# Performance work log

Hardware: AMD Instinct MI355X
Metric: run time of the kernel (lower is better)

Reference implementation:

```python
import jax, jax.numpy as jnp
import numpy as np

N = 100000      # nodes
E = 1600000     # edges (before self-loops)
IN = 64         # in_channels
HID = 16        # hidden_channels
HEADS = 4       # num_heads
G = 512         # number of graphs in batch
SLOPE = 0.2     # GATConv leaky_relu negative_slope


def setup_inputs() -> dict:
    key = jax.random.key(0)
    ks = jax.random.split(key, 12)
    s = 0.1
    x = jax.random.normal(ks[0], (N, IN), jnp.float32)
    edge_index = jax.random.randint(ks[1], (2, E), 0, N, dtype=jnp.int64)
    batch = jnp.sort(jax.random.randint(ks[2], (N,), 0, G, dtype=jnp.int64))
    W1 = jax.random.normal(ks[3], (IN, HEADS * HID), jnp.float32) * s
    a1_src = jax.random.normal(ks[4], (HEADS, HID), jnp.float32) * s
    a1_dst = jax.random.normal(ks[5], (HEADS, HID), jnp.float32) * s
    b1 = jnp.zeros((HEADS * HID,), jnp.float32)
    W2 = jax.random.normal(ks[6], (HEADS * HID, HID), jnp.float32) * s
    a2_src = jax.random.normal(ks[7], (1, HID), jnp.float32) * s
    a2_dst = jax.random.normal(ks[8], (1, HID), jnp.float32) * s
    b2 = jnp.zeros((HID,), jnp.float32)
    Wc = jax.random.normal(ks[9], (HID, 1), jnp.float32) * s
    bc = jnp.zeros((1,), jnp.float32)
    return dict(x=x, edge_index=edge_index, batch=batch, W1=W1, a1_src=a1_src,
                a1_dst=a1_dst, b1=b1, W2=W2, a2_src=a2_src, a2_dst=a2_dst,
                b2=b2, Wc=Wc, bc=bc)


def gat_layer(x, src, dst, W, a_s, a_d, bias, heads, out_ch, concat):
    # PyG GATConv: linear -> per-edge attention logits -> segment softmax over dst -> scatter aggregate
    n = x.shape[0]
    h = (x @ W).reshape(n, heads, out_ch)              # [N, H, C]
    al_s = jnp.sum(h * a_s, axis=-1)                   # [N, H]
    al_d = jnp.sum(h * a_d, axis=-1)                   # [N, H]
    e = al_s[src] + al_d[dst]                          # [E, H]
    e = jnp.where(e > 0, e, SLOPE * e)                 # leaky_relu
    m = jax.ops.segment_max(e, dst, num_segments=n)    # per-dst max (self-loops ensure non-empty)
    p = jnp.exp(e - m[dst])
    denom = jax.ops.segment_sum(p, dst, num_segments=n)
    alpha = p / (denom[dst] + 1e-16)                   # [E, H]
    out = jax.ops.segment_sum(h[src] * alpha[:, :, None], dst, num_segments=n)  # [N, H, C]
    out = out.reshape(n, heads * out_ch) if concat else out.mean(axis=1)
    return out + bias


def reference(x, edge_index, batch, W1, a1_src, a1_dst, b1, W2, a2_src, a2_dst, b2, Wc, bc):
    loops = jnp.arange(N, dtype=edge_index.dtype)      # GATConv add_self_loops=True
    src = jnp.concatenate([edge_index[0], loops])
    dst = jnp.concatenate([edge_index[1], loops])
    h = jax.nn.elu(gat_layer(x, src, dst, W1, a1_src, a1_dst, b1, HEADS, HID, True))
    # dropout inactive (eval mode)
    h = jax.nn.elu(gat_layer(h, src, dst, W2, a2_src, a2_dst, b2, 1, HID, False))
    counts = jax.ops.segment_sum(jnp.ones((N,), h.dtype), batch, num_segments=G)
    pooled = jax.ops.segment_sum(h, batch, num_segments=G) / jnp.maximum(counts, 1.0)[:, None]
    return pooled @ Wc + bc
```

## Files before the change

kernel.cpp:

```cpp
#include <hip/hip_runtime.h>
#include <hip/hip_fp16.h>
#include <hip/hip_fp8.h>

#define N_NODES 100000
#define N_EDGES 1600000
#define ET      (N_EDGES + N_NODES)
#define NG      512
#define SLOPE   0.2f

#define BKT_SHIFT 9
#define NB_B   ((N_NODES + 511) / 512)
#define CHUNK_A 8192
#define NBLK_A ((ET + CHUNK_A - 1) / CHUNK_A)
#define H1B    ((N_NODES + 255) / 256)

typedef _Float16 half8_t __attribute__((ext_vector_type(8)));
typedef float    f32x4_t __attribute__((ext_vector_type(4)));

__global__ __launch_bounds__(256) void k_prep(
    const float* __restrict__ x, const float* __restrict__ W1,
    const float* __restrict__ a1s, const float* __restrict__ a1d,
    const int* __restrict__ ei,
    __hip_fp8_e4m3* __restrict__ h1, float* __restrict__ al1s, float* __restrict__ al1d,
    int* __restrict__ bsize)
{
    __shared__ float Wl[64 * 64];
    __shared__ float asf[64], adf[64];
    __shared__ int hcnt[NB_B];
    int tid = threadIdx.x;

    if (blockIdx.x >= H1B) {
        for (int i = tid; i < NB_B; i += 256) hcnt[i] = 0;
        __syncthreads();
        int base = (blockIdx.x - H1B) * CHUNK_A;
        int m = min(CHUNK_A, ET - base);
        for (int i = tid; i < m; i += 256) {
            int eid = base + i;
            int d = (eid < N_EDGES) ? ei[N_EDGES + eid] : (eid - N_EDGES);
            atomicAdd(&hcnt[d >> BKT_SHIFT], 1);
        }
        __syncthreads();
        for (int i = tid; i < NB_B; i += 256)
            if (hcnt[i]) atomicAdd(&bsize[i], hcnt[i]);
        return;
    }

    for (int i = tid; i < 64 * 64; i += 256) Wl[i] = W1[i];
    if (tid < 64) { asf[tid] = a1s[tid]; adf[tid] = a1d[tid]; }
    __syncthreads();

    int wv = tid >> 6, lane = tid & 63;
    int m = lane & 15, q = lane >> 4;

    half8_t bf[4][2];
#pragma unroll
    for (int t = 0; t < 4; ++t)
#pragma unroll
        for (int s = 0; s < 2; ++s) {
            half8_t b;
#pragma unroll
            for (int j = 0; j < 8; ++j)
                b[j] = (_Float16)Wl[(s * 32 + q * 8 + j) * 64 + t * 16 + m];
            bf[t][s] = b;
        }

    for (int it = 0; it < 4; ++it) {
        int node0 = blockIdx.x * 256 + wv * 64 + it * 16;
        int node = node0 + m;
        half8_t av0 = {}, av1 = {};
        if (node < N_NODES) {
            const float4* xr = (const float4*)(x + (long long)node * 64);
            float4 p0 = xr[q * 2], p1 = xr[q * 2 + 1];
            float4 p2 = xr[q * 2 + 8], p3 = xr[q * 2 + 9];
            av0[0] = (_Float16)p0.x; av0[1] = (_Float16)p0.y;
            av0[2] = (_Float16)p0.z; av0[3] = (_Float16)p0.w;
            av0[4] = (_Float16)p1.x; av0[5] = (_Float16)p1.y;
            av0[6] = (_Float16)p1.z; av0[7] = (_Float16)p1.w;
            av1[0] = (_Float16)p2.x; av1[1] = (_Float16)p2.y;
            av1[2] = (_Float16)p2.z; av1[3] = (_Float16)p2.w;
            av1[4] = (_Float16)p3.x; av1[5] = (_Float16)p3.y;
            av1[6] = (_Float16)p3.z; av1[7] = (_Float16)p3.w;
        }
        f32x4_t acc[4] = {{0,0,0,0},{0,0,0,0},{0,0,0,0},{0,0,0,0}};
#pragma unroll
        for (int t = 0; t < 4; ++t) {
            acc[t] = __builtin_amdgcn_mfma_f32_16x16x32_f16(av0, bf[t][0], acc[t], 0, 0, 0);
            acc[t] = __builtin_amdgcn_mfma_f32_16x16x32_f16(av1, bf[t][1], acc[t], 0, 0, 0);
        }
#pragma unroll
        for (int r = 0; r < 4; ++r) {
            int nr = node0 + q * 4 + r;
            bool ok = nr < N_NODES;
#pragma unroll
            for (int t = 0; t < 4; ++t) {
                float v = acc[t][r];
                if (ok) h1[(long long)nr * 64 + t * 16 + m] = __hip_fp8_e4m3(v);
                float ps = v * asf[t * 16 + m];
                float pd = v * adf[t * 16 + m];
                ps += __shfl_xor(ps, 1); ps += __shfl_xor(ps, 2);
                ps += __shfl_xor(ps, 4); ps += __shfl_xor(ps, 8);
                pd += __shfl_xor(pd, 1); pd += __shfl_xor(pd, 2);
                pd += __shfl_xor(pd, 4); pd += __shfl_xor(pd, 8);
                if (ok && m == t) { al1s[nr * 4 + t] = ps; al1d[nr * 4 + t] = pd; }
            }
        }
    }
}

__global__ __launch_bounds__(256) void k_scanB(const int* __restrict__ bsize,
                                               int* __restrict__ bbase, int* __restrict__ bcur)
{
    __shared__ int tmp[256];
    int tid = threadIdx.x;
    int v = (tid < NB_B) ? bsize[tid] : 0;
    tmp[tid] = v;
    __syncthreads();
    for (int off = 1; off < 256; off <<= 1) {
        int t = (tid >= off) ? tmp[tid - off] : 0;
        __syncthreads();
        tmp[tid] += t;
        __syncthreads();
    }
    if (tid < NB_B) { int e = tmp[tid] - v; bbase[tid] = e; bcur[tid] = e; }
}

__global__ __launch_bounds__(1024) void k_passA(const int* __restrict__ ei,
                                                int* __restrict__ bcur, unsigned int* __restrict__ ebuf)
{
    __shared__ unsigned int stage[CHUNK_A];
    __shared__ unsigned char sbin[CHUNK_A];
    __shared__ int hist[NB_B];
    __shared__ int binst[NB_B];
    __shared__ int resv[NB_B];
    __shared__ int cur[NB_B];
    __shared__ int tmp[1024];
    int tid = threadIdx.x;
    int base = blockIdx.x * CHUNK_A;
    int m = min(CHUNK_A, ET - base);
    for (int i = tid; i < NB_B; i += 1024) hist[i] = 0;
    __syncthreads();
    for (int i = tid; i < m; i += 1024) {
        int eid = base + i;
        int d = (eid < N_EDGES) ? ei[N_EDGES + eid] : (eid - N_EDGES);
        atomicAdd(&hist[d >> BKT_SHIFT], 1);
    }
    __syncthreads();
    int v = (tid < NB_B) ? hist[tid] : 0;
    tmp[tid] = v;
    __syncthreads();
    for (int off = 1; off < 1024; off <<= 1) {
        int t = (tid >= off) ? tmp[tid - off] : 0;
        __syncthreads();
        tmp[tid] += t;
        __syncthreads();
    }
    if (tid < NB_B) {
        int e = tmp[tid] - v;
        binst[tid] = e;
        cur[tid] = e;
        resv[tid] = v ? atomicAdd(&bcur[tid], v) : 0;
    }
    __syncthreads();
    for (int i = tid; i < m; i += 1024) {
        int eid = base + i;
        int s, d;
        if (eid < N_EDGES) { s = ei[eid]; d = ei[N_EDGES + eid]; }
        else               { s = eid - N_EDGES; d = s; }
        int b = d >> BKT_SHIFT;
        int pos = atomicAdd(&cur[b], 1);
        stage[pos] = ((unsigned int)(d & 511) << 17) | (unsigned int)s;
        sbin[pos] = (unsigned char)b;
    }
    __syncthreads();
    for (int i = tid; i < m; i += 1024) {
        int b = sbin[i];
        ebuf[resv[b] + (i - binst[b])] = stage[i];
    }
}

__global__ __launch_bounds__(1024) void k_passB(
    const unsigned int* __restrict__ ebuf, const int* __restrict__ bbase,
    const int* __restrict__ bsize,
    int* __restrict__ csr, int* __restrict__ offs, int* __restrict__ deg)
{
    __shared__ int ldeg[512];
    __shared__ int lofs[512];
    __shared__ int lcur[512];
    int tid = threadIdx.x;
    int b = blockIdx.x;
    int nb0 = b << BKT_SHIFT;
    int nn = min(512, N_NODES - nb0);
    int gbase = bbase[b], cnt = bsize[b];
    if (tid < 512) ldeg[tid] = 0;
    __syncthreads();
    for (int i = tid; i < cnt; i += 1024)
        atomicAdd(&ldeg[ebuf[gbase + i] >> 17], 1);
    __syncthreads();
    int v = 0;
    if (tid < 512) { v = ldeg[tid]; lofs[tid] = v; }
    __syncthreads();
    for (int off = 1; off < 512; off <<= 1) {
        int t = (tid >= off && tid < 512) ? lofs[tid - off] : 0;
        __syncthreads();
        if (tid < 512) lofs[tid] += t;
        __syncthreads();
    }
    if (tid < 512) {
        int e = lofs[tid] - v;
        lcur[tid] = e;
        if (tid < nn) { offs[nb0 + tid] = gbase + e; deg[nb0 + tid] = v; }
    }
    __syncthreads();
    for (int i = tid; i < cnt; i += 1024) {
        unsigned int ev = ebuf[gbase + i];
        int dl = ev >> 17, s = (int)(ev & 0x1FFFF);
        int p = atomicAdd(&lcur[dl], 1);
        csr[gbase + p] = s;
    }
}

__global__ __launch_bounds__(256) void k_agg1(
    const int* __restrict__ offs, const int* __restrict__ deg, const int* __restrict__ csr,
    const __hip_fp8_e4m3* __restrict__ h1, const float* __restrict__ al1s, const float* __restrict__ al1d,
    const float* __restrict__ b1, __half* __restrict__ h1bg)
{
    __shared__ int   sarr[4][64];
    __shared__ float warr[4][4 * 72];
    __shared__ __align__(16) float h1b[4][64];
    int tid = threadIdx.x;
    int wv = tid >> 6, lane = tid & 63;
    int eslot = lane >> 4;
    int cq = lane & 15;
    int h = cq >> 2;
    int cq4 = cq * 4;
    int node = blockIdx.x * 4 + wv;
    int st = offs[node], dg = deg[node];
    const float4 ald4 = *(const float4*)(al1d + node * 4);
    float b1l = b1[lane];
    const char* __restrict__ h1c = (const char*)h1;

    float a0 = 0.f, a1 = 0.f, a2 = 0.f, a3 = 0.f, den = 0.f;
    for (int base = 0; base < dg; base += 64) {
        int m = min(64, dg - base);
        int s = 0;
        float w0 = 0.f, w1 = 0.f, w2 = 0.f, w3 = 0.f;
        if (lane < m) {
            s = csr[st + base + lane];
            const float4 as4 = *(const float4*)(al1s + s * 4);
            float e0 = as4.x + ald4.x; e0 = e0 > 0.f ? e0 : SLOPE * e0;
            float e1 = as4.y + ald4.y; e1 = e1 > 0.f ? e1 : SLOPE * e1;
            float e2 = as4.z + ald4.z; e2 = e2 > 0.f ? e2 : SLOPE * e2;
            float e3 = as4.w + ald4.w; e3 = e3 > 0.f ? e3 : SLOPE * e3;
            w0 = __expf(e0); w1 = __expf(e1); w2 = __expf(e2); w3 = __expf(e3);
        }
        sarr[wv][lane] = s << 6;
        warr[wv][0 * 72 + lane] = w0;
        warr[wv][1 * 72 + lane] = w1;
        warr[wv][2 * 72 + lane] = w2;
        warr[wv][3 * 72 + lane] = w3;
        int m4 = (m + 3) & ~3;
#pragma unroll 4
        for (int j0 = 0; j0 < m4; j0 += 4) {
            int j = j0 + eslot;
            int off = sarr[wv][j] + cq4;
            float wgt = warr[wv][h * 72 + j];
            unsigned int pk = *(const unsigned int*)(h1c + off);
            a0 = fmaf(wgt, __builtin_amdgcn_cvt_f32_fp8(pk, 0), a0);
            a1 = fmaf(wgt, __builtin_amdgcn_cvt_f32_fp8(pk, 1), a1);
            a2 = fmaf(wgt, __builtin_amdgcn_cvt_f32_fp8(pk, 2), a2);
            a3 = fmaf(wgt, __builtin_amdgcn_cvt_f32_fp8(pk, 3), a3);
            den += wgt;
        }
    }
    a0 += __shfl_xor(a0, 16); a0 += __shfl_xor(a0, 32);
    a1 += __shfl_xor(a1, 16); a1 += __shfl_xor(a1, 32);
    a2 += __shfl_xor(a2, 16); a2 += __shfl_xor(a2, 32);
    a3 += __shfl_xor(a3, 16); a3 += __shfl_xor(a3, 32);
    den += __shfl_xor(den, 16); den += __shfl_xor(den, 32);
    if (lane < 16)
        *(float4*)&h1b[wv][cq4] = make_float4(a0, a1, a2, a3);
    float denc = __shfl(den, (lane >> 4) << 2);
    float v = h1b[wv][lane] / (denc + 1e-16f) + b1l;
    v = v > 0.f ? v : __expf(v) - 1.f;
    h1bg[(long long)node * 64 + lane] = __float2half_rn(v);
}

__global__ __launch_bounds__(256) void k_mid(
    const __half* __restrict__ h1bg, const float* __restrict__ W2,
    const float* __restrict__ a2s, const float* __restrict__ a2d,
    __half* __restrict__ h2, float* __restrict__ al2s, float* __restrict__ al2d)
{
    __shared__ float W2l[64 * 16];
    int tid = threadIdx.x;
    for (int i = tid; i < 64 * 16; i += 256) W2l[i] = W2[i];
    __syncthreads();
    int wv = tid >> 6, lane = tid & 63;
    int m = lane & 15, q = lane >> 4;
    half8_t bf[2];
#pragma unroll
    for (int s = 0; s < 2; ++s) {
        half8_t b;
#pragma unroll
        for (int j = 0; j < 8; ++j)
            b[j] = (_Float16)W2l[(s * 32 + q * 8 + j) * 16 + m];
        bf[s] = b;
    }
    int node0 = blockIdx.x * 64 + wv * 16;
    half8_t av0 = {}, av1 = {};
    if (node0 + m < N_NODES) {
        const __half* ar = h1bg + (long long)(node0 + m) * 64;
        av0 = *(const half8_t*)(ar + q * 8);
        av1 = *(const half8_t*)(ar + 32 + q * 8);
    }
    f32x4_t acc = {0, 0, 0, 0};
    acc = __builtin_amdgcn_mfma_f32_16x16x32_f16(av0, bf[0], acc, 0, 0, 0);
    acc = __builtin_amdgcn_mfma_f32_16x16x32_f16(av1, bf[1], acc, 0, 0, 0);
    float a2sm = a2s[m], a2dm = a2d[m];
#pragma unroll
    for (int r = 0; r < 4; ++r) {
        int nr = node0 + q * 4 + r;
        bool ok = nr < N_NODES;
        float v = acc[r];
        if (ok) h2[nr * 16 + m] = __float2half_rn(v);
        float ps = v * a2sm, pd = v * a2dm;
        ps += __shfl_xor(ps, 1); ps += __shfl_xor(ps, 2);
        ps += __shfl_xor(ps, 4); ps += __shfl_xor(ps, 8);
        pd += __shfl_xor(pd, 1); pd += __shfl_xor(pd, 2);
        pd += __shfl_xor(pd, 4); pd += __shfl_xor(pd, 8);
        if (ok && m == 0) { al2s[nr] = ps; al2d[nr] = pd; }
    }
}

__global__ __launch_bounds__(256) void k_agg2(
    const int* __restrict__ offs, const int* __restrict__ deg, const int* __restrict__ csr,
    const __half* __restrict__ h2, const float* __restrict__ al2s, const float* __restrict__ al2d,
    const float* __restrict__ b2, float* __restrict__ hout)
{
    __shared__ int   sarr[4][64];
    __shared__ float warr[4][64];
    int tid = threadIdx.x;
    int wv = tid >> 6, lane = tid & 63;
    int ec = lane >> 3, cc = lane & 7;
    int node = blockIdx.x * 4 + wv;
    int st = offs[node], dg = deg[node];
    float ald = al2d[node];
    const __half2* __restrict__ h2v = (const __half2*)h2;

    float a0 = 0.f, a1 = 0.f, den = 0.f;
    for (int base = 0; base < dg; base += 64) {
        int m = min(64, dg - base);
        int s = 0; float wl = 0.f;
        if (lane < m) {
            s = csr[st + base + lane];
            float e = al2s[s] + ald;
            e = e > 0.f ? e : SLOPE * e;
            wl = __expf(e);
        }
        sarr[wv][lane] = s;
        warr[wv][lane] = wl;
        float t = wl;
#pragma unroll
        for (int x = 1; x < 64; x <<= 1) t += __shfl_xor(t, x);
        den += t;
        int m8 = (m + 7) & ~7;
#pragma unroll 2
        for (int j0 = 0; j0 < m8; j0 += 8) {
            int j = j0 + ec;
            int s2i = sarr[wv][j];
            float wgt = warr[wv][j];
            __half2 hv = h2v[s2i * 8 + cc];
            a0 = fmaf(__low2float(hv), wgt, a0);
            a1 = fmaf(__high2float(hv), wgt, a1);
        }
    }
    a0 += __shfl_xor(a0, 8);  a1 += __shfl_xor(a1, 8);
    a0 += __shfl_xor(a0, 16); a1 += __shfl_xor(a1, 16);
    a0 += __shfl_xor(a0, 32); a1 += __shfl_xor(a1, 32);
    if (lane < 8) {
        float inv = 1.f / (den + 1e-16f);
        float v0 = a0 * inv + b2[2 * cc];
        float v1 = a1 * inv + b2[2 * cc + 1];
        v0 = v0 > 0.f ? v0 : __expf(v0) - 1.f;
        v1 = v1 > 0.f ? v1 : __expf(v1) - 1.f;
        ((float2*)hout)[node * 8 + cc] = make_float2(v0, v1);
    }
}

__global__ __launch_bounds__(256) void k_pool(
    const float* __restrict__ hout, const int* __restrict__ batch,
    const float* __restrict__ Wc, const float* __restrict__ bc, float* __restrict__ out)
{
    __shared__ float red[16][17];
    __shared__ int bnd[2];
    int g = blockIdx.x;
    int t = threadIdx.x, c = t & 15, slot = t >> 4;
    if (t < 2) {
        int key = g + t;
        int lo = 0, hi = N_NODES;
        while (lo < hi) { int mid = (lo + hi) >> 1; if (batch[mid] < key) lo = mid + 1; else hi = mid; }
        bnd[t] = lo;
    }
    __syncthreads();
    int s = bnd[0], e = bnd[1];
    float sum = 0.f;
    for (int n = s + slot; n < e; n += 16)
        sum += hout[n * 16 + c];
    red[slot][c] = sum;
    __syncthreads();
    if (t < 16) {
        float tot = 0.f;
#pragma unroll
        for (int k = 0; k < 16; ++k) tot += red[k][t];
        float cnt = fmaxf((float)(e - s), 1.0f);
        float pc = (tot / cnt) * Wc[t];
        pc += __shfl_xor(pc, 1); pc += __shfl_xor(pc, 2);
        pc += __shfl_xor(pc, 4); pc += __shfl_xor(pc, 8);
        if (t == 0) out[g] = pc + bc[0];
    }
}

extern "C" void kernel_launch(void* const* d_in, const int* in_sizes, int n_in,
                              void* d_out, int out_size, void* d_ws, size_t ws_size,
                              hipStream_t stream)
{
    const float* x    = (const float*)d_in[0];
    const int*   ei   = (const int*)d_in[1];
    const int*   batc = (const int*)d_in[2];
    const float* W1   = (const float*)d_in[3];
    const float* a1s  = (const float*)d_in[4];
    const float* a1d  = (const float*)d_in[5];
    const float* b1   = (const float*)d_in[6];
    const float* W2   = (const float*)d_in[7];
    const float* a2s  = (const float*)d_in[8];
    const float* a2d  = (const float*)d_in[9];
    const float* b2   = (const float*)d_in[10];
    const float* Wc   = (const float*)d_in[11];
    const float* bc   = (const float*)d_in[12];
    float* out = (float*)d_out;

    char* ws = (char*)d_ws;
    size_t off = 0;
    auto carveB = [&](size_t bytes) {
        void* p = ws + off;
        off += ((bytes + 15) & ~(size_t)15);
        return p;
    };
    auto carve = [&](size_t elems) { return carveB(elems * 4); };
    int*   bsize  = (int*)  carve(NB_B);
    size_t zero_bytes = off;
    int*   bbase  = (int*)  carve(NB_B);
    int*   bcur   = (int*)  carve(NB_B);
    unsigned int* ebuf = (unsigned int*)carve(ET);
    int*   csr    = (int*)  carve(ET);
    int*   offs   = (int*)  carve(N_NODES);
    int*   deg    = (int*)  carve(N_NODES);
    __hip_fp8_e4m3* h1 = (__hip_fp8_e4m3*)carveB((size_t)N_NODES * 64);
    float* al1s   = (float*)carve((size_t)N_NODES * 4);
    float* al1d   = (float*)carve((size_t)N_NODES * 4);
    __half* h1bg  = (__half*)carveB((size_t)N_NODES * 64 * 2);
    __half* h2    = (__half*)carveB((size_t)N_NODES * 16 * 2);
    float* al2s   = (float*)carve(N_NODES);
    float* al2d   = (float*)carve(N_NODES);
    float* hout   = (float*)carve((size_t)N_NODES * 16);

    hipMemsetAsync(d_ws, 0, zero_bytes, stream);

    k_prep <<<H1B + NBLK_A, 256, 0, stream>>>(x, W1, a1s, a1d, ei, h1, al1s, al1d, bsize);
    k_scanB<<<1, 256, 0, stream>>>(bsize, bbase, bcur);
    k_passA<<<NBLK_A, 1024, 0, stream>>>(ei, bcur, ebuf);
    k_passB<<<NB_B, 1024, 0, stream>>>(ebuf, bbase, bsize, csr, offs, deg);
    k_agg1 <<<N_NODES / 4, 256, 0, stream>>>(offs, deg, csr, h1, al1s, al1d, b1, h1bg);
    k_mid  <<<(N_NODES + 63) / 64, 256, 0, stream>>>(h1bg, W2, a2s, a2d, h2, al2s, al2d);
    k_agg2 <<<N_NODES / 4, 256, 0, stream>>>(offs, deg, csr, h2, al2s, al2d,
                                             b2, hout);
    k_pool <<<NG, 256, 0, stream>>>(hout, batc, Wc, bc, out);
}
```

Measured before the change: 260.8 us.

## Fuse CSR build passes with fixed bucket capacity and fuse mid/pool into aggregations

Replaces the count/scan/scatter sequence with a single pass that scatters edges into fixed-capacity per-bucket regions (BCAP), removing the global histogram and scan kernels. It also fuses the layer-2 linear transform and attention logits into the layer-1 aggregation, which removes the h1bg round trip through memory. Mean pooling becomes atomic accumulation inside agg2, followed by a tiny classifier kernel. The trade-offs are more launches avoided against a risk of bucket overflow if a bucket exceeds BCAP, nondeterministic float atomics, and extra per-block W2 loading in agg1.

```diff
diff --git a/kernel.cpp b/kernel.cpp
--- a/kernel.cpp
+++ b/kernel.cpp
@@ -10,43 +10,77 @@
 
 #define BKT_SHIFT 9
 #define NB_B   ((N_NODES + 511) / 512)
+#define BCAP   10240
 #define CHUNK_A 8192
 #define NBLK_A ((ET + CHUNK_A - 1) / CHUNK_A)
-#define H1B    ((N_NODES + 255) / 256)
+#define H1B4   ((N_NODES + 1023) / 1024)
 
 typedef _Float16 half8_t __attribute__((ext_vector_type(8)));
 typedef float    f32x4_t __attribute__((ext_vector_type(4)));
-
-__global__ __launch_bounds__(256) void k_prep(
+typedef float    f32x2_t __attribute__((ext_vector_type(2)));
+
+__global__ __launch_bounds__(1024) void k_prepA(
     const float* __restrict__ x, const float* __restrict__ W1,
     const float* __restrict__ a1s, const float* __restrict__ a1d,
     const int* __restrict__ ei,
-    __hip_fp8_e4m3* __restrict__ h1, float* __restrict__ al1s, float* __restrict__ al1d,
-    int* __restrict__ bsize)
-{
-    __shared__ float Wl[64 * 64];
-    __shared__ float asf[64], adf[64];
-    __shared__ int hcnt[NB_B];
+    int* __restrict__ gcnt, unsigned int* __restrict__ ebuf,
+    __hip_fp8_e4m3* __restrict__ h1, float* __restrict__ al1s, float* __restrict__ al1d)
+{
+    __shared__ union U {
+        struct { float Wl[64 * 64]; float asf[64]; float adf[64]; } p;
+        struct { unsigned int stage[CHUNK_A]; unsigned char sbin[CHUNK_A];
+                 int hist[NB_B]; int binst[NB_B]; int resv[NB_B]; int cur[NB_B];
+                 int tmp[1024]; } a;
+    } u;
     int tid = threadIdx.x;
 
-    if (blockIdx.x >= H1B) {
-        for (int i = tid; i < NB_B; i += 256) hcnt[i] = 0;
-        __syncthreads();
-        int base = (blockIdx.x - H1B) * CHUNK_A;
+    if (blockIdx.x < NBLK_A) {
+        int base = blockIdx.x * CHUNK_A;
         int m = min(CHUNK_A, ET - base);
-        for (int i = tid; i < m; i += 256) {
+        for (int i = tid; i < NB_B; i += 1024) u.a.hist[i] = 0;
+        __syncthreads();
+        for (int i = tid; i < m; i += 1024) {
             int eid = base + i;
             int d = (eid < N_EDGES) ? ei[N_EDGES + eid] : (eid - N_EDGES);
-            atomicAdd(&hcnt[d >> BKT_SHIFT], 1);
-        }
-        __syncthreads();
-        for (int i = tid; i < NB_B; i += 256)
-            if (hcnt[i]) atomicAdd(&bsize[i], hcnt[i]);
+            atomicAdd(&u.a.hist[d >> BKT_SHIFT], 1);
+        }
+        __syncthreads();
+        int v = (tid < NB_B) ? u.a.hist[tid] : 0;
+        u.a.tmp[tid] = v;
+        __syncthreads();
+        for (int off = 1; off < 1024; off <<= 1) {
+            int t = (tid >= off) ? u.a.tmp[tid - off] : 0;
+            __syncthreads();
+            u.a.tmp[tid] += t;
+            __syncthreads();
+        }
+        if (tid < NB_B) {
+            int e = u.a.tmp[tid] - v;
+            u.a.binst[tid] = e;
+            u.a.cur[tid] = e;
+            u.a.resv[tid] = v ? atomicAdd(&gcnt[tid], v) : 0;
+        }
+        __syncthreads();
+        for (int i = tid; i < m; i += 1024) {
+            int eid = base + i;
+            int s, d;
+            if (eid < N_EDGES) { s = ei[eid]; d = ei[N_EDGES + eid]; }
+            else               { s = eid - N_EDGES; d = s; }
+            int b = d >> BKT_SHIFT;
+            int pos = atomicAdd(&u.a.cur[b], 1);
+            u.a.stage[pos] = ((unsigned int)(d & 511) << 17) | (unsigned int)s;
+            u.a.sbin[pos] = (unsigned char)b;
+        }
+        __syncthreads();
+        for (int i = tid; i < m; i += 1024) {
+            int b = u.a.sbin[i];
+            ebuf[b * BCAP + u.a.resv[b] + (i - u.a.binst[b])] = u.a.stage[i];
+        }
         return;
     }
 
-    for (int i = tid; i < 64 * 64; i += 256) Wl[i] = W1[i];
-    if (tid < 64) { asf[tid] = a1s[tid]; adf[tid] = a1d[tid]; }
+    for (int i = tid; i < 64 * 64; i += 1024) u.p.Wl[i] = W1[i];
+    if (tid < 64) { u.p.asf[tid] = a1s[tid]; u.p.adf[tid] = a1d[tid]; }
     __syncthreads();
 
     int wv = tid >> 6, lane = tid & 63;
@@ -60,12 +94,13 @@
             half8_t b;
 #pragma unroll
             for (int j = 0; j < 8; ++j)
-                b[j] = (_Float16)Wl[(s * 32 + q * 8 + j) * 64 + t * 16 + m];
+                b[j] = (_Float16)u.p.Wl[(s * 32 + q * 8 + j) * 64 + t * 16 + m];
             bf[t][s] = b;
         }
 
+    int nodebase = (blockIdx.x - NBLK_A) * 1024 + wv * 64;
     for (int it = 0; it < 4; ++it) {
-        int node0 = blockIdx.x * 256 + wv * 64 + it * 16;
+        int node0 = nodebase + it * 16;
         int node = node0 + m;
         half8_t av0 = {}, av1 = {};
         if (node < N_NODES) {
@@ -95,8 +130,8 @@
             for (int t = 0; t < 4; ++t) {
                 float v = acc[t][r];
                 if (ok) h1[(long long)nr * 64 + t * 16 + m] = __hip_fp8_e4m3(v);
-                float ps = v * asf[t * 16 + m];
-                float pd = v * adf[t * 16 + m];
+                float ps = v * u.p.asf[t * 16 + m];
+                float pd = v * u.p.adf[t * 16 + m];
                 ps += __shfl_xor(ps, 1); ps += __shfl_xor(ps, 2);
                 ps += __shfl_xor(ps, 4); ps += __shfl_xor(ps, 8);
                 pd += __shfl_xor(pd, 1); pd += __shfl_xor(pd, 2);
@@ -107,80 +142,8 @@
     }
 }
 
-__global__ __launch_bounds__(256) void k_scanB(const int* __restrict__ bsize,
-                                               int* __restrict__ bbase, int* __restrict__ bcur)
-{
-    __shared__ int tmp[256];
-    int tid = threadIdx.x;
-    int v = (tid < NB_B) ? bsize[tid] : 0;
-    tmp[tid] = v;
-    __syncthreads();
-    for (int off = 1; off < 256; off <<= 1) {
-        int t = (tid >= off) ? tmp[tid - off] : 0;
-        __syncthreads();
-        tmp[tid] += t;
-        __syncthreads();
-    }
-    if (tid < NB_B) { int e = tmp[tid] - v; bbase[tid] = e; bcur[tid] = e; }
-}
-
-__global__ __launch_bounds__(1024) void k_passA(const int* __restrict__ ei,
-                                                int* __restrict__ bcur, unsigned int* __restrict__ ebuf)
-{
-    __shared__ unsigned int stage[CHUNK_A];
-    __shared__ unsigned char sbin[CHUNK_A];
-    __shared__ int hist[NB_B];
-    __shared__ int binst[NB_B];
-    __shared__ int resv[NB_B];
-    __shared__ int cur[NB_B];
-    __shared__ int tmp[1024];
-    int tid = threadIdx.x;
-    int base = blockIdx.x * CHUNK_A;
-    int m = min(CHUNK_A, ET - base);
-    for (int i = tid; i < NB_B; i += 1024) hist[i] = 0;
-    __syncthreads();
-    for (int i = tid; i < m; i += 1024) {
-        int eid = base + i;
-        int d = (eid < N_EDGES) ? ei[N_EDGES + eid] : (eid - N_EDGES);
-        atomicAdd(&hist[d >> BKT_SHIFT], 1);
-    }
-    __syncthreads();
-    int v = (tid < NB_B) ? hist[tid] : 0;
-    tmp[tid] = v;
-    __syncthreads();
-    for (int off = 1; off < 1024; off <<= 1) {
-        int t = (tid >= off) ? tmp[tid - off] : 0;
-        __syncthreads();
-        tmp[tid] += t;
-        __syncthreads();
-    }
-    if (tid < NB_B) {
-        int e = tmp[tid] - v;
-        binst[tid] = e;
-        cur[tid] = e;
-        resv[tid] = v ? atomicAdd(&bcur[tid], v) : 0;
-    }
-    __syncthreads();
-    for (int i = tid; i < m; i += 1024) {
-        int eid = base + i;
-        int s, d;
-        if (eid < N_EDGES) { s = ei[eid]; d = ei[N_EDGES + eid]; }
-        else               { s = eid - N_EDGES; d = s; }
-        int b = d >> BKT_SHIFT;
-        int pos = atomicAdd(&cur[b], 1);
-        stage[pos] = ((unsigned int)(d & 511) << 17) | (unsigned int)s;
-        sbin[pos] = (unsigned char)b;
-    }
-    __syncthreads();
-    for (int i = tid; i < m; i += 1024) {
-        int b = sbin[i];
-        ebuf[resv[b] + (i - binst[b])] = stage[i];
-    }
-}
-
 __global__ __launch_bounds__(1024) void k_passB(
-    const unsigned int* __restrict__ ebuf, const int* __restrict__ bbase,
-    const int* __restrict__ bsize,
+    const unsigned int* __restrict__ ebuf, const int* __restrict__ gcnt,
     int* __restrict__ csr, int* __restrict__ offs, int* __restrict__ deg)
 {
     __shared__ int ldeg[512];
@@ -190,7 +153,7 @@
     int b = blockIdx.x;
     int nb0 = b << BKT_SHIFT;
     int nn = min(512, N_NODES - nb0);
-    int gbase = bbase[b], cnt = bsize[b];
+    int gbase = b * BCAP, cnt = gcnt[b];
     if (tid < 512) ldeg[tid] = 0;
     __syncthreads();
     for (int i = tid; i < cnt; i += 1024)
@@ -222,16 +185,24 @@
 __global__ __launch_bounds__(256) void k_agg1(
     const int* __restrict__ offs, const int* __restrict__ deg, const int* __restrict__ csr,
     const __hip_fp8_e4m3* __restrict__ h1, const float* __restrict__ al1s, const float* __restrict__ al1d,
-    const float* __restrict__ b1, __half* __restrict__ h1bg)
+    const float* __restrict__ b1, const float* __restrict__ W2,
+    const float* __restrict__ a2s, const float* __restrict__ a2d,
+    __half* __restrict__ h2, float* __restrict__ al2s, float* __restrict__ al2d)
 {
     __shared__ int   sarr[4][64];
     __shared__ float warr[4][4 * 72];
     __shared__ __align__(16) float h1b[4][64];
+    __shared__ __align__(16) float W2t[16][66];
+    __shared__ float a2sl[16], a2dl[16];
     int tid = threadIdx.x;
+    for (int i = tid; i < 64 * 16; i += 256) W2t[i & 15][i >> 4] = W2[i];
+    if (tid < 16) { a2sl[tid] = a2s[tid]; a2dl[tid] = a2d[tid]; }
+    __syncthreads();
+
     int wv = tid >> 6, lane = tid & 63;
     int eslot = lane >> 4;
     int cq = lane & 15;
-    int h = cq >> 2;
+    int hh = cq >> 2;
     int cq4 = cq * 4;
     int node = blockIdx.x * 4 + wv;
     int st = offs[node], dg = deg[node];
@@ -239,7 +210,8 @@
     float b1l = b1[lane];
     const char* __restrict__ h1c = (const char*)h1;
 
-    float a0 = 0.f, a1 = 0.f, a2 = 0.f, a3 = 0.f, den = 0.f;
+    f32x2_t a01 = {0.f, 0.f}, a23 = {0.f, 0.f};
+    float den = 0.f;
     for (int base = 0; base < dg; base += 64) {
         int m = min(64, dg - base);
         int s = 0;
@@ -263,81 +235,59 @@
         for (int j0 = 0; j0 < m4; j0 += 4) {
             int j = j0 + eslot;
             int off = sarr[wv][j] + cq4;
-            float wgt = warr[wv][h * 72 + j];
+            float wgt = warr[wv][hh * 72 + j];
             unsigned int pk = *(const unsigned int*)(h1c + off);
-            a0 = fmaf(wgt, __builtin_amdgcn_cvt_f32_fp8(pk, 0), a0);
-            a1 = fmaf(wgt, __builtin_amdgcn_cvt_f32_fp8(pk, 1), a1);
-            a2 = fmaf(wgt, __builtin_amdgcn_cvt_f32_fp8(pk, 2), a2);
-            a3 = fmaf(wgt, __builtin_amdgcn_cvt_f32_fp8(pk, 3), a3);
+            f32x2_t wg2 = {wgt, wgt};
+            a01 = __builtin_elementwise_fma(wg2, __builtin_amdgcn_cvt_pk_f32_fp8((int)pk, false), a01);
+            a23 = __builtin_elementwise_fma(wg2, __builtin_amdgcn_cvt_pk_f32_fp8((int)pk, true),  a23);
             den += wgt;
         }
     }
-    a0 += __shfl_xor(a0, 16); a0 += __shfl_xor(a0, 32);
-    a1 += __shfl_xor(a1, 16); a1 += __shfl_xor(a1, 32);
-    a2 += __shfl_xor(a2, 16); a2 += __shfl_xor(a2, 32);
-    a3 += __shfl_xor(a3, 16); a3 += __shfl_xor(a3, 32);
-    den += __shfl_xor(den, 16); den += __shfl_xor(den, 32);
+    a01.x += __shfl_xor(a01.x, 16); a01.x += __shfl_xor(a01.x, 32);
+    a01.y += __shfl_xor(a01.y, 16); a01.y += __shfl_xor(a01.y, 32);
+    a23.x += __shfl_xor(a23.x, 16); a23.x += __shfl_xor(a23.x, 32);
+    a23.y += __shfl_xor(a23.y, 16); a23.y += __shfl_xor(a23.y, 32);
+    den   += __shfl_xor(den, 16);   den   += __shfl_xor(den, 32);
     if (lane < 16)
-        *(float4*)&h1b[wv][cq4] = make_float4(a0, a1, a2, a3);
+        *(float4*)&h1b[wv][cq4] = make_float4(a01.x, a01.y, a23.x, a23.y);
     float denc = __shfl(den, (lane >> 4) << 2);
+    __builtin_amdgcn_wave_barrier();
     float v = h1b[wv][lane] / (denc + 1e-16f) + b1l;
     v = v > 0.f ? v : __expf(v) - 1.f;
-    h1bg[(long long)node * 64 + lane] = __float2half_rn(v);
-}
-
-__global__ __launch_bounds__(256) void k_mid(
-    const __half* __restrict__ h1bg, const float* __restrict__ W2,
-    const float* __restrict__ a2s, const float* __restrict__ a2d,
-    __half* __restrict__ h2, float* __restrict__ al2s, float* __restrict__ al2d)
-{
-    __shared__ float W2l[64 * 16];
-    int tid = threadIdx.x;
-    for (int i = tid; i < 64 * 16; i += 256) W2l[i] = W2[i];
-    __syncthreads();
-    int wv = tid >> 6, lane = tid & 63;
-    int m = lane & 15, q = lane >> 4;
-    half8_t bf[2];
-#pragma unroll
-    for (int s = 0; s < 2; ++s) {
-        half8_t b;
-#pragma unroll
-        for (int j = 0; j < 8; ++j)
-            b[j] = (_Float16)W2l[(s * 32 + q * 8 + j) * 16 + m];
-        bf[s] = b;
-    }
-    int node0 = blockIdx.x * 64 + wv * 16;
-    half8_t av0 = {}, av1 = {};
-    if (node0 + m < N_NODES) {
-        const __half* ar = h1bg + (long long)(node0 + m) * 64;
-        av0 = *(const half8_t*)(ar + q * 8);
-        av1 = *(const half8_t*)(ar + 32 + q * 8);
-    }
-    f32x4_t acc = {0, 0, 0, 0};
-    acc = __builtin_amdgcn_mfma_f32_16x16x32_f16(av0, bf[0], acc, 0, 0, 0);
-    acc = __builtin_amdgcn_mfma_f32_16x16x32_f16(av1, bf[1], acc, 0, 0, 0);
-    float a2sm = a2s[m], a2dm = a2d[m];
-#pragma unroll
-    for (int r = 0; r < 4; ++r) {
-        int nr = node0 + q * 4 + r;
-        bool ok = nr < N_NODES;
-        float v = acc[r];
-        if (ok) h2[nr * 16 + m] = __float2half_rn(v);
-        float ps = v * a2sm, pd = v * a2dm;
-        ps += __shfl_xor(ps, 1); ps += __shfl_xor(ps, 2);
-        ps += __shfl_xor(ps, 4); ps += __shfl_xor(ps, 8);
-        pd += __shfl_xor(pd, 1); pd += __shfl_xor(pd, 2);
-        pd += __shfl_xor(pd, 4); pd += __shfl_xor(pd, 8);
-        if (ok && m == 0) { al2s[nr] = ps; al2d[nr] = pd; }
-    }
+    h1b[wv][lane] = v;
+    __builtin_amdgcn_wave_barrier();
+
+    int c2 = lane & 15, slot = lane >> 4;
+    f32x2_t acc2 = {0.f, 0.f};
+#pragma unroll
+    for (int i = 0; i < 8; ++i) {
+        int k = slot * 16 + i * 2;
+        f32x2_t hv  = *(const f32x2_t*)&h1b[wv][k];
+        f32x2_t wv2 = *(const f32x2_t*)&W2t[c2][k];
+        acc2 = __builtin_elementwise_fma(hv, wv2, acc2);
+    }
+    float h2val = acc2.x + acc2.y;
+    h2val += __shfl_xor(h2val, 16);
+    h2val += __shfl_xor(h2val, 32);
+    float ps2 = h2val * a2sl[c2];
+    float pd2 = h2val * a2dl[c2];
+    ps2 += __shfl_xor(ps2, 1); ps2 += __shfl_xor(ps2, 2);
+    ps2 += __shfl_xor(ps2, 4); ps2 += __shfl_xor(ps2, 8);
+    pd2 += __shfl_xor(pd2, 1); pd2 += __shfl_xor(pd2, 2);
+    pd2 += __shfl_xor(pd2, 4); pd2 += __shfl_xor(pd2, 8);
+    if (lane < 16) h2[node * 16 + c2] = __float2half_rn(h2val);
+    if (lane == 0) { al2s[node] = ps2; al2d[node] = pd2; }
 }
 
 __global__ __launch_bounds__(256) void k_agg2(
     const int* __restrict__ offs, const int* __restrict__ deg, const int* __restrict__ csr,
     const __half* __restrict__ h2, const float* __restrict__ al2s, const float* __restrict__ al2d,
-    const float* __restrict__ b2, float* __restrict__ hout)
-{
-    __shared__ int   sarr[4][64];
-    __shared__ float warr[4][64];
+    const float* __restrict__ b2, const int* __restrict__ batch, float* __restrict__ pooled)
+{
+    __shared__ int    sarr[4][64];
+    __shared__ float  warr[4][64];
+    __shared__ float2 pl[4][8];
+    __shared__ int    gl[4];
     int tid = threadIdx.x;
     int wv = tid >> 6, lane = tid & 63;
     int ec = lane >> 3, cc = lane & 7;
@@ -382,41 +332,43 @@
         float v1 = a1 * inv + b2[2 * cc + 1];
         v0 = v0 > 0.f ? v0 : __expf(v0) - 1.f;
         v1 = v1 > 0.f ? v1 : __expf(v1) - 1.f;
-        ((float2*)hout)[node * 8 + cc] = make_float2(v0, v1);
-    }
-}
-
-__global__ __launch_bounds__(256) void k_pool(
-    const float* __restrict__ hout, const int* __restrict__ batch,
+        pl[wv][cc] = make_float2(v0, v1);
+    }
+    if (lane == 0) gl[wv] = batch[node];
+    __syncthreads();
+    if (wv == 0 && lane < 8) {
+        int g0 = gl[0], g3 = gl[3];
+        if (g0 == g3) {
+            float2 s0 = pl[0][lane], s1 = pl[1][lane], s2 = pl[2][lane], s3 = pl[3][lane];
+            atomicAdd(&pooled[g0 * 16 + 2 * lane],     s0.x + s1.x + s2.x + s3.x);
+            atomicAdd(&pooled[g0 * 16 + 2 * lane + 1], s0.y + s1.y + s2.y + s3.y);
+        } else {
+#pragma unroll
+            for (int nd = 0; nd < 4; ++nd) {
+                float2 s = pl[nd][lane];
+                atomicAdd(&pooled[gl[nd] * 16 + 2 * lane],     s.x);
+                atomicAdd(&pooled[gl[nd] * 16 + 2 * lane + 1], s.y);
+            }
+        }
+    }
+}
+
+__global__ __launch_bounds__(256) void k_cls(
+    const float* __restrict__ pooled, const int* __restrict__ batch,
     const float* __restrict__ Wc, const float* __restrict__ bc, float* __restrict__ out)
 {
-    __shared__ float red[16][17];
-    __shared__ int bnd[2];
-    int g = blockIdx.x;
-    int t = threadIdx.x, c = t & 15, slot = t >> 4;
-    if (t < 2) {
-        int key = g + t;
-        int lo = 0, hi = N_NODES;
-        while (lo < hi) { int mid = (lo + hi) >> 1; if (batch[mid] < key) lo = mid + 1; else hi = mid; }
-        bnd[t] = lo;
-    }
-    __syncthreads();
-    int s = bnd[0], e = bnd[1];
-    float sum = 0.f;
-    for (int n = s + slot; n < e; n += 16)
-        sum += hout[n * 16 + c];
-    red[slot][c] = sum;
-    __syncthreads();
-    if (t < 16) {
-        float tot = 0.f;
-#pragma unroll
-        for (int k = 0; k < 16; ++k) tot += red[k][t];
-        float cnt = fmaxf((float)(e - s), 1.0f);
-        float pc = (tot / cnt) * Wc[t];
-        pc += __shfl_xor(pc, 1); pc += __shfl_xor(pc, 2);
-        pc += __shfl_xor(pc, 4); pc += __shfl_xor(pc, 8);
-        if (t == 0) out[g] = pc + bc[0];
-    }
+    int g = blockIdx.x * 256 + threadIdx.x;
+    if (g >= NG) return;
+    int lo = 0, hi = N_NODES;
+    while (lo < hi) { int mid = (lo + hi) >> 1; if (batch[mid] < g) lo = mid + 1; else hi = mid; }
+    int s = lo;
+    lo = 0; hi = N_NODES;
+    while (lo < hi) { int mid = (lo + hi) >> 1; if (batch[mid] < g + 1) lo = mid + 1; else hi = mid; }
+    float cnt = fmaxf((float)(lo - s), 1.0f);
+    float acc = 0.f;
+#pragma unroll
+    for (int c = 0; c < 16; ++c) acc += pooled[g * 16 + c] * Wc[c];
+    out[g] = acc / cnt + bc[0];
 }
 
 extern "C" void kernel_launch(void* const* d_in, const int* in_sizes, int n_in,
@@ -446,32 +398,26 @@
         return p;
     };
     auto carve = [&](size_t elems) { return carveB(elems * 4); };
-    int*   bsize  = (int*)  carve(NB_B);
+    int*   gcnt   = (int*)  carve(NB_B);
+    float* pooled = (float*)carve((size_t)NG * 16);
     size_t zero_bytes = off;
-    int*   bbase  = (int*)  carve(NB_B);
-    int*   bcur   = (int*)  carve(NB_B);
-    unsigned int* ebuf = (unsigned int*)carve(ET);
-    int*   csr    = (int*)  carve(ET);
+    unsigned int* ebuf = (unsigned int*)carve((size_t)NB_B * BCAP);
+    int*   csr    = (int*)  carve((size_t)NB_B * BCAP);
     int*   offs   = (int*)  carve(N_NODES);
     int*   deg    = (int*)  carve(N_NODES);
     __hip_fp8_e4m3* h1 = (__hip_fp8_e4m3*)carveB((size_t)N_NODES * 64);
     float* al1s   = (float*)carve((size_t)N_NODES * 4);
     float* al1d   = (float*)carve((size_t)N_NODES * 4);
-    __half* h1bg  = (__half*)carveB((size_t)N_NODES * 64 * 2);
     __half* h2    = (__half*)carveB((size_t)N_NODES * 16 * 2);
     float* al2s   = (float*)carve(N_NODES);
     float* al2d   = (float*)carve(N_NODES);
-    float* hout   = (float*)carve((size_t)N_NODES * 16);
 
     hipMemsetAsync(d_ws, 0, zero_bytes, stream);
 
-    k_prep <<<H1B + NBLK_A, 256, 0, stream>>>(x, W1, a1s, a1d, ei, h1, al1s, al1d, bsize);
-    k_scanB<<<1, 256, 0, stream>>>(bsize, bbase, bcur);
-    k_passA<<<NBLK_A, 1024, 0, stream>>>(ei, bcur, ebuf);
-    k_passB<<<NB_B, 1024, 0, stream>>>(ebuf, bbase, bsize, csr, offs, deg);
-    k_agg1 <<<N_NODES / 4, 256, 0, stream>>>(offs, deg, csr, h1, al1s, al1d, b1, h1bg);
-    k_mid  <<<(N_NODES + 63) / 64, 256, 0, stream>>>(h1bg, W2, a2s, a2d, h2, al2s, al2d);
-    k_agg2 <<<N_NODES / 4, 256, 0, stream>>>(offs, deg, csr, h2, al2s, al2d,
-                                             b2, hout);
-    k_pool <<<NG, 256, 0, stream>>>(hout, batc, Wc, bc, out);
-}
+    k_prepA<<<NBLK_A + H1B4, 1024, 0, stream>>>(x, W1, a1s, a1d, ei, gcnt, ebuf, h1, al1s, al1d);
+    k_passB<<<NB_B, 1024, 0, stream>>>(ebuf, gcnt, csr, offs, deg);
+    k_agg1 <<<N_NODES / 4, 256, 0, stream>>>(offs, deg, csr, h1, al1s, al1d, b1,
+                                             W2, a2s, a2d, h2, al2s, al2d);
+    k_agg2 <<<N_NODES / 4, 256, 0, stream>>>(offs, deg, csr, h2, al2s, al2d, b2, batc, pooled);
+    k_cls  <<<NG / 256, 256, 0, stream>>>(pooled, batc, Wc, bc, out);
+}
```

Result: slower. 280.3 us (+7.5%).

## Replace bucketed two-pass CSR build with per-node degree atomics and global scatter

Applied to the files above, without the earlier changes.

CSR construction no longer goes through destination buckets and LDS staging. It now counts per-node degrees with global atomics, computes offsets with a three-kernel hierarchical scan, and scatters sources with one global atomic per edge. This drops the intermediate edge buffer and its second pass, but adds kernel launches and heavily contended global atomics with uncoalesced writes. Separately, k_prep moves to 1024-thread blocks, and k_agg2 accumulates the softmax denominator per lane inside the gather loop instead of doing a full wave reduction per chunk.

```diff
diff --git a/kernel.cpp b/kernel.cpp
--- a/kernel.cpp
+++ b/kernel.cpp
@@ -8,44 +8,37 @@
 #define NG      512
 #define SLOPE   0.2f
 
-#define BKT_SHIFT 9
-#define NB_B   ((N_NODES + 511) / 512)
 #define CHUNK_A 8192
 #define NBLK_A ((ET + CHUNK_A - 1) / CHUNK_A)
-#define H1B    ((N_NODES + 255) / 256)
+#define H1B4   ((N_NODES + 1023) / 1024)
+#define NBLK_S ((N_NODES + 1023) / 1024)
 
 typedef _Float16 half8_t __attribute__((ext_vector_type(8)));
 typedef float    f32x4_t __attribute__((ext_vector_type(4)));
 
-__global__ __launch_bounds__(256) void k_prep(
+__global__ __launch_bounds__(1024) void k_prep(
     const float* __restrict__ x, const float* __restrict__ W1,
     const float* __restrict__ a1s, const float* __restrict__ a1d,
     const int* __restrict__ ei,
-    __hip_fp8_e4m3* __restrict__ h1, float* __restrict__ al1s, float* __restrict__ al1d,
-    int* __restrict__ bsize)
+    int* __restrict__ deg,
+    __hip_fp8_e4m3* __restrict__ h1, float* __restrict__ al1s, float* __restrict__ al1d)
 {
     __shared__ float Wl[64 * 64];
     __shared__ float asf[64], adf[64];
-    __shared__ int hcnt[NB_B];
-    int tid = threadIdx.x;
-
-    if (blockIdx.x >= H1B) {
-        for (int i = tid; i < NB_B; i += 256) hcnt[i] = 0;
-        __syncthreads();
-        int base = (blockIdx.x - H1B) * CHUNK_A;
+    int tid = threadIdx.x;
+
+    if (blockIdx.x < NBLK_A) {
+        int base = blockIdx.x * CHUNK_A;
         int m = min(CHUNK_A, ET - base);
-        for (int i = tid; i < m; i += 256) {
+        for (int i = tid; i < m; i += 1024) {
             int eid = base + i;
             int d = (eid < N_EDGES) ? ei[N_EDGES + eid] : (eid - N_EDGES);
-            atomicAdd(&hcnt[d >> BKT_SHIFT], 1);
-        }
-        __syncthreads();
-        for (int i = tid; i < NB_B; i += 256)
-            if (hcnt[i]) atomicAdd(&bsize[i], hcnt[i]);
+            atomicAdd(&deg[d], 1);
+        }
         return;
     }
 
-    for (int i = tid; i < 64 * 64; i += 256) Wl[i] = W1[i];
+    for (int i = tid; i < 64 * 64; i += 1024) Wl[i] = W1[i];
     if (tid < 64) { asf[tid] = a1s[tid]; adf[tid] = a1d[tid]; }
     __syncthreads();
 
@@ -64,8 +57,9 @@
             bf[t][s] = b;
         }
 
+    int nodebase = (blockIdx.x - NBLK_A) * 1024 + wv * 64;
     for (int it = 0; it < 4; ++it) {
-        int node0 = blockIdx.x * 256 + wv * 64 + it * 16;
+        int node0 = nodebase + it * 16;
         int node = node0 + m;
         half8_t av0 = {}, av1 = {};
         if (node < N_NODES) {
@@ -107,45 +101,13 @@
     }
 }
 
-__global__ __launch_bounds__(256) void k_scanB(const int* __restrict__ bsize,
-                                               int* __restrict__ bbase, int* __restrict__ bcur)
-{
-    __shared__ int tmp[256];
-    int tid = threadIdx.x;
-    int v = (tid < NB_B) ? bsize[tid] : 0;
-    tmp[tid] = v;
-    __syncthreads();
-    for (int off = 1; off < 256; off <<= 1) {
-        int t = (tid >= off) ? tmp[tid - off] : 0;
-        __syncthreads();
-        tmp[tid] += t;
-        __syncthreads();
-    }
-    if (tid < NB_B) { int e = tmp[tid] - v; bbase[tid] = e; bcur[tid] = e; }
-}
-
-__global__ __launch_bounds__(1024) void k_passA(const int* __restrict__ ei,
-                                                int* __restrict__ bcur, unsigned int* __restrict__ ebuf)
-{
-    __shared__ unsigned int stage[CHUNK_A];
-    __shared__ unsigned char sbin[CHUNK_A];
-    __shared__ int hist[NB_B];
-    __shared__ int binst[NB_B];
-    __shared__ int resv[NB_B];
-    __shared__ int cur[NB_B];
+__global__ __launch_bounds__(1024) void k_scanA(
+    const int* __restrict__ deg, int* __restrict__ offs, int* __restrict__ bsum)
+{
     __shared__ int tmp[1024];
     int tid = threadIdx.x;
-    int base = blockIdx.x * CHUNK_A;
-    int m = min(CHUNK_A, ET - base);
-    for (int i = tid; i < NB_B; i += 1024) hist[i] = 0;
-    __syncthreads();
-    for (int i = tid; i < m; i += 1024) {
-        int eid = base + i;
-        int d = (eid < N_EDGES) ? ei[N_EDGES + eid] : (eid - N_EDGES);
-        atomicAdd(&hist[d >> BKT_SHIFT], 1);
-    }
-    __syncthreads();
-    int v = (tid < NB_B) ? hist[tid] : 0;
+    int gid = blockIdx.x * 1024 + tid;
+    int v = (gid < N_NODES) ? deg[gid] : 0;
     tmp[tid] = v;
     __syncthreads();
     for (int off = 1; off < 1024; off <<= 1) {
@@ -154,68 +116,50 @@
         tmp[tid] += t;
         __syncthreads();
     }
-    if (tid < NB_B) {
-        int e = tmp[tid] - v;
-        binst[tid] = e;
-        cur[tid] = e;
-        resv[tid] = v ? atomicAdd(&bcur[tid], v) : 0;
-    }
-    __syncthreads();
-    for (int i = tid; i < m; i += 1024) {
+    if (gid < N_NODES) offs[gid] = tmp[tid] - v;
+    if (tid == 1023) bsum[blockIdx.x] = tmp[tid];
+}
+
+__global__ __launch_bounds__(128) void k_scanB2(
+    const int* __restrict__ bsum, int* __restrict__ bpre)
+{
+    __shared__ int tmp[128];
+    int tid = threadIdx.x;
+    int v = (tid < NBLK_S) ? bsum[tid] : 0;
+    tmp[tid] = v;
+    __syncthreads();
+    for (int off = 1; off < 128; off <<= 1) {
+        int t = (tid >= off) ? tmp[tid - off] : 0;
+        __syncthreads();
+        tmp[tid] += t;
+        __syncthreads();
+    }
+    if (tid < NBLK_S) bpre[tid] = tmp[tid] - v;
+}
+
+__global__ __launch_bounds__(1024) void k_fix(
+    int* __restrict__ offs, int* __restrict__ cur, const int* __restrict__ bpre)
+{
+    int gid = blockIdx.x * 1024 + threadIdx.x;
+    if (gid < N_NODES) {
+        int o = offs[gid] + bpre[blockIdx.x];
+        offs[gid] = o;
+        cur[gid] = o;
+    }
+}
+
+__global__ __launch_bounds__(1024) void k_scatter(
+    const int* __restrict__ ei, int* __restrict__ cur, int* __restrict__ csr)
+{
+    int base = blockIdx.x * CHUNK_A;
+    int m = min(CHUNK_A, ET - base);
+    for (int i = threadIdx.x; i < m; i += 1024) {
         int eid = base + i;
         int s, d;
         if (eid < N_EDGES) { s = ei[eid]; d = ei[N_EDGES + eid]; }
         else               { s = eid - N_EDGES; d = s; }
-        int b = d >> BKT_SHIFT;
-        int pos = atomicAdd(&cur[b], 1);
-        stage[pos] = ((unsigned int)(d & 511) << 17) | (unsigned int)s;
-        sbin[pos] = (unsigned char)b;
-    }
-    __syncthreads();
-    for (int i = tid; i < m; i += 1024) {
-        int b = sbin[i];
-        ebuf[resv[b] + (i - binst[b])] = stage[i];
-    }
-}
-
-__global__ __launch_bounds__(1024) void k_passB(
-    const unsigned int* __restrict__ ebuf, const int* __restrict__ bbase,
-    const int* __restrict__ bsize,
-    int* __restrict__ csr, int* __restrict__ offs, int* __restrict__ deg)
-{
-    __shared__ int ldeg[512];
-    __shared__ int lofs[512];
-    __shared__ int lcur[512];
-    int tid = threadIdx.x;
-    int b = blockIdx.x;
-    int nb0 = b << BKT_SHIFT;
-    int nn = min(512, N_NODES - nb0);
-    int gbase = bbase[b], cnt = bsize[b];
-    if (tid < 512) ldeg[tid] = 0;
-    __syncthreads();
-    for (int i = tid; i < cnt; i += 1024)
-        atomicAdd(&ldeg[ebuf[gbase + i] >> 17], 1);
-    __syncthreads();
-    int v = 0;
-    if (tid < 512) { v = ldeg[tid]; lofs[tid] = v; }
-    __syncthreads();
-    for (int off = 1; off < 512; off <<= 1) {
-        int t = (tid >= off && tid < 512) ? lofs[tid - off] : 0;
-        __syncthreads();
-        if (tid < 512) lofs[tid] += t;
-        __syncthreads();
-    }
-    if (tid < 512) {
-        int e = lofs[tid] - v;
-        lcur[tid] = e;
-        if (tid < nn) { offs[nb0 + tid] = gbase + e; deg[nb0 + tid] = v; }
-    }
-    __syncthreads();
-    for (int i = tid; i < cnt; i += 1024) {
-        unsigned int ev = ebuf[gbase + i];
-        int dl = ev >> 17, s = (int)(ev & 0x1FFFF);
-        int p = atomicAdd(&lcur[dl], 1);
-        csr[gbase + p] = s;
+        int pos = atomicAdd(&cur[d], 1);
+        csr[pos] = s;
     }
 }
 
@@ -358,10 +302,6 @@
         }
         sarr[wv][lane] = s;
         warr[wv][lane] = wl;
-        float t = wl;
-#pragma unroll
-        for (int x = 1; x < 64; x <<= 1) t += __shfl_xor(t, x);
-        den += t;
         int m8 = (m + 7) & ~7;
 #pragma unroll 2
         for (int j0 = 0; j0 < m8; j0 += 8) {
@@ -371,11 +311,12 @@
             __half2 hv = h2v[s2i * 8 + cc];
             a0 = fmaf(__low2float(hv), wgt, a0);
             a1 = fmaf(__high2float(hv), wgt, a1);
-        }
-    }
-    a0 += __shfl_xor(a0, 8);  a1 += __shfl_xor(a1, 8);
-    a0 += __shfl_xor(a0, 16); a1 += __shfl_xor(a1, 16);
-    a0 += __shfl_xor(a0, 32); a1 += __shfl_xor(a1, 32);
+            den += wgt;
+        }
+    }
+    a0 += __shfl_xor(a0, 8);  a1 += __shfl_xor(a1, 8);  den += __shfl_xor(den, 8);
+    a0 += __shfl_xor(a0, 16); a1 += __shfl_xor(a1, 16); den += __shfl_xor(den, 16);
+    a0 += __shfl_xor(a0, 32); a1 += __shfl_xor(a1, 32); den += __shfl_xor(den, 32);
     if (lane < 8) {
         float inv = 1.f / (den + 1e-16f);
         float v0 = a0 * inv + b2[2 * cc];
@@ -446,14 +387,13 @@
         return p;
     };
     auto carve = [&](size_t elems) { return carveB(elems * 4); };
-    int*   bsize  = (int*)  carve(NB_B);
+    int*   deg    = (int*)  carve(N_NODES);
     size_t zero_bytes = off;
-    int*   bbase  = (int*)  carve(NB_B);
-    int*   bcur   = (int*)  carve(NB_B);
-    unsigned int* ebuf = (unsigned int*)carve(ET);
+    int*   offs   = (int*)  carve(N_NODES);
+    int*   cur    = (int*)  carve(N_NODES);
+    int*   bsum   = (int*)  carve(NBLK_S);
+    int*   bpre   = (int*)  carve(NBLK_S);
     int*   csr    = (int*)  carve(ET);
-    int*   offs   = (int*)  carve(N_NODES);
-    int*   deg    = (int*)  carve(N_NODES);
     __hip_fp8_e4m3* h1 = (__hip_fp8_e4m3*)carveB((size_t)N_NODES * 64);
     float* al1s   = (float*)carve((size_t)N_NODES * 4);
     float* al1d   = (float*)carve((size_t)N_NODES * 4);
@@ -465,13 +405,13 @@
 
     hipMemsetAsync(d_ws, 0, zero_bytes, stream);
 
-    k_prep <<<H1B + NBLK_A, 256, 0, stream>>>(x, W1, a1s, a1d, ei, h1, al1s, al1d, bsize);
-    k_scanB<<<1, 256, 0, stream>>>(bsize, bbase, bcur);
-    k_passA<<<NBLK_A, 1024, 0, stream>>>(ei, bcur, ebuf);
-    k_passB<<<NB_B, 1024, 0, stream>>>(ebuf, bbase, bsize, csr, offs, deg);
-    k_agg1 <<<N_NODES / 4, 256, 0, stream>>>(offs, deg, csr, h1, al1s, al1d, b1, h1bg);
-    k_mid  <<<(N_NODES + 63) / 64, 256, 0, stream>>>(h1bg, W2, a2s, a2d, h2, al2s, al2d);
-    k_agg2 <<<N_NODES / 4, 256, 0, stream>>>(offs, deg, csr, h2, al2s, al2d,
-                                             b2, hout);
-    k_pool <<<NG, 256, 0, stream>>>(hout, batc, Wc, bc, out);
-}
+    k_prep   <<<NBLK_A + H1B4, 1024, 0, stream>>>(x, W1, a1s, a1d, ei, deg, h1, al1s, al1d);
+    k_scanA  <<<NBLK_S, 1024, 0, stream>>>(deg, offs, bsum);
+    k_scanB2 <<<1, 128, 0, stream>>>(bsum, bpre);
+    k_fix    <<<NBLK_S, 1024, 0, stream>>>(offs, cur, bpre);
+    k_scatter<<<NBLK_A, 1024, 0, stream>>>(ei, cur, csr);
+    k_agg1   <<<N_NODES / 4, 256, 0, stream>>>(offs, deg, csr, h1, al1s, al1d, b1, h1bg);
+    k_mid    <<<(N_NODES + 63) / 64, 256, 0, stream>>>(h1bg, W2, a2s, a2d, h2, al2s, al2d);
+    k_agg2   <<<N_NODES / 4, 256, 0, stream>>>(offs, deg, csr, h2, al2s, al2d, b2, hout);
+    k_pool   <<<NG, 256, 0, stream>>>(hout, batc, Wc, bc, out);
+}
```

Measured after the change: 368.4 us. 1.41x slower.
